# Performance work log

Hardware: AMD Instinct MI355X
Metric: run time of the kernel (lower is better)

Reference implementation:

```python
import jax, jax.numpy as jnp
import numpy as np

C = 16          # image channels (scaled from 1 for production-scale traffic)
GX = 36         # CORTIAL_WIDTH_COUNT
GY = 36         # CORTIAL_HEIGHT_COUNT
RF = 24         # receptive field size
IMG = 64        # image H = W
GAMMA_E = 0.9
GAMMA_I = 0.9


def setup_inputs() -> dict:
    key = jax.random.key(0)
    ks = jax.random.split(key, 7)
    x = jax.random.normal(ks[0], (C, IMG, IMG), dtype=jnp.float32)
    prev_activity = jax.random.uniform(ks[1], (C, GX, GY), dtype=jnp.float32)
    afferent_weights = jax.random.normal(ks[2], (C, GX, GY, RF, RF), dtype=jnp.float32) * 0.05
    ex_lateral_weights = jax.random.normal(ks[3], (C, GX, GY, GX, GY), dtype=jnp.float32) * 0.05
    in_lateral_weights = jax.random.normal(ks[4], (C, GX, GY, GX, GY), dtype=jnp.float32) * 0.05
    rx = jnp.sort(jax.random.randint(ks[5], (GX,), 0, IMG - RF + 1, dtype=jnp.int32))
    ry = jnp.sort(jax.random.randint(ks[6], (GY,), 0, IMG - RF + 1, dtype=jnp.int32))
    return {
        "x": x,
        "prev_activity": prev_activity,
        "afferent_weights": afferent_weights,
        "ex_lateral_weights": ex_lateral_weights,
        "in_lateral_weights": in_lateral_weights,
        "rx": rx,
        "ry": ry,
    }


def reference(x, prev_activity, afferent_weights, ex_lateral_weights, in_lateral_weights, rx, ry):
    # Gather all receptive-field patches at once: patches[c,i,j,u,v] = x[c, rx[i]+u, ry[j]+v]
    u = jnp.arange(RF)
    ix = (rx[:, None] + u)[:, None, :, None]   # [GX,1,RF,1]
    iy = (ry[:, None] + u)[None, :, None, :]   # [1,GY,1,RF]
    patches = x[:, ix, iy]                     # [C,GX,GY,RF,RF]

    # afferent_activation[:,i,j] = sum(patch * W_a[:,i,j]) (scalar broadcast across channels)
    aff = jnp.einsum('cijuv,cijuv->ij', patches, afferent_weights)
    # lateral activations: sum(prev[:,i,j] * W[:,i,j]) over all elements
    exc = jnp.einsum('cij,cijxy->ij', prev_activity, ex_lateral_weights)
    inh = jnp.einsum('cij,cijxy->ij', prev_activity, in_lateral_weights)

    total = aff + GAMMA_E * exc - GAMMA_I * inh   # [GX,GY]
    activity = jnp.maximum(total, 0.0)            # clamp(min=0) sigmoid approximation
    return jnp.broadcast_to(activity[None, :, :], (C, GX, GY))
```

## Files before the change

kernel.cpp:

```cpp
#include <hip/hip_runtime.h>


constexpr int C   = 16;
constexpr int GX  = 36;
constexpr int GY  = 36;
constexpr int RF  = 24;
constexpr int IMG = 64;
constexpr int GG  = GX * GY;
constexpr int RR  = RF * RF;
constexpr int SPLIT = 4;
constexpr int CPB   = C / SPLIT;

typedef float f4 __attribute__((ext_vector_type(4)));

__global__ __launch_bounds__(256)
void cortex_phase1(const float* __restrict__ x,
                   const float* __restrict__ prev,
                   const float* __restrict__ affW,
                   const float* __restrict__ exW,
                   const float* __restrict__ inW,
                   const int*   __restrict__ rx,
                   const int*   __restrict__ ry,
                   float* __restrict__ partial)
{
    const int bid   = blockIdx.x;
    const int ij    = bid % GG;
    const int split = bid / GG;
    const int cs    = split * CPB;
    const int i = ij / GY;
    const int j = ij - i * GY;
    const int t = threadIdx.x;

    const int rxi = rx[i];
    const int ryj = ry[j];

    float acc = 0.0f;

    if (t < RR / 4) {
        const int u  = t / (RF / 4);
        const int v0 = 4 * (t - u * (RF / 4));
        f4 w[CPB];
        #pragma unroll
        for (int cc = 0; cc < CPB; ++cc) {
            const int c = cs + cc;
            w[cc] = __builtin_nontemporal_load(
                (const f4*)(affW + ((size_t)c * GG + ij) * RR) + t);
        }
        #pragma unroll
        for (int cc = 0; cc < CPB; ++cc) {
            const int c = cs + cc;
            const float* xp = x + ((c * IMG + rxi + u) * IMG + ryj + v0);
            acc = fmaf(w[cc].x, xp[0], acc);
            acc = fmaf(w[cc].y, xp[1], acc);
            acc = fmaf(w[cc].z, xp[2], acc);
            acc = fmaf(w[cc].w, xp[3], acc);
        }
    }

    float d[CPB] = {0.0f, 0.0f, 0.0f, 0.0f};
    for (int k = t; k < GG / 4; k += 256) {
        f4 e[CPB], h[CPB];
        #pragma unroll
        for (int cc = 0; cc < CPB; ++cc) {
            const size_t base = ((size_t)(cs + cc) * GG + ij) * GG;
            e[cc] = __builtin_nontemporal_load((const f4*)(exW + base) + k);
            h[cc] = __builtin_nontemporal_load((const f4*)(inW + base) + k);
        }
        #pragma unroll
        for (int cc = 0; cc < CPB; ++cc)
            d[cc] += (e[cc].x + e[cc].y + e[cc].z + e[cc].w)
                   - (h[cc].x + h[cc].y + h[cc].z + h[cc].w);
    }
    {
        float lat = 0.0f;
        #pragma unroll
        for (int cc = 0; cc < CPB; ++cc)
            lat = fmaf(prev[(cs + cc) * GG + ij], d[cc], lat);
        acc = fmaf(0.9f, lat, acc);
    }

    for (int off = 32; off > 0; off >>= 1)
        acc += __shfl_down(acc, off, 64);

    __shared__ float sred[4];
    const int wave = t >> 6;
    const int lane = t & 63;
    if (lane == 0) sred[wave] = acc;
    __syncthreads();
    if (t == 0)
        partial[split * GG + ij] = sred[0] + sred[1] + sred[2] + sred[3];
}

__global__ __launch_bounds__(256)
void cortex_phase2(const float* __restrict__ partial, float* __restrict__ out)
{
    const int ij = blockIdx.x * blockDim.x + threadIdx.x;
    if (ij < GG) {
        const float tot = partial[ij] + partial[GG + ij]
                        + partial[2 * GG + ij] + partial[3 * GG + ij];
        const float a = fmaxf(tot, 0.0f);
        #pragma unroll
        for (int c = 0; c < C; ++c)
            out[c * GG + ij] = a;
    }
}

extern "C" void kernel_launch(void* const* d_in, const int* in_sizes, int n_in,
                              void* d_out, int out_size, void* d_ws, size_t ws_size,
                              hipStream_t stream) {
    const float* x     = (const float*)d_in[0];
    const float* prev  = (const float*)d_in[1];
    const float* affW  = (const float*)d_in[2];
    const float* exW   = (const float*)d_in[3];
    const float* inW   = (const float*)d_in[4];
    const int*   rx    = (const int*)d_in[5];
    const int*   ry    = (const int*)d_in[6];
    float* out     = (float*)d_out;
    float* partial = (float*)d_ws;

    cortex_phase1<<<GG * SPLIT, 256, 0, stream>>>(x, prev, affW, exW, inW, rx, ry, partial);
    cortex_phase2<<<(GG + 255) / 256, 256, 0, stream>>>(partial, out);
}
```

Baseline: 245.9 us.

## Flatten per-block work into uniform thread-strided loops with fewer channel splits

Halves the channel split so each block handles 8 channels, and flattens the afferent and lateral loads into one index space spread across all 256 threads instead of leaving most threads idle in the afferent part. Per-row pointers and signed prev-scaled coefficients are precomputed in shared memory, so excitatory and inhibitory rows are handled by one loop with eight independent 16-byte loads in flight per thread. This is meant to improve memory-level parallelism and lane utilization on a bandwidth-bound kernel, at the cost of integer divisions, a shared-memory sync and fewer blocks.

```diff
diff --git a/kernel.cpp b/kernel.cpp
--- a/kernel.cpp
+++ b/kernel.cpp
@@ -8,7 +8,7 @@
 constexpr int IMG = 64;
 constexpr int GG  = GX * GY;
 constexpr int RR  = RF * RF;
-constexpr int SPLIT = 4;
+constexpr int SPLIT = 2;
 constexpr int CPB   = C / SPLIT;
 
 typedef float f4 __attribute__((ext_vector_type(4)));
@@ -23,60 +23,78 @@
                    const int*   __restrict__ ry,
                    float* __restrict__ partial)
 {
-    const int bid   = blockIdx.x;
-    const int ij    = bid % GG;
-    const int split = bid / GG;
-    const int cs    = split * CPB;
+    const int bid  = blockIdx.x;
+    const int ij   = bid % GG;
+    const int half = bid / GG;
+    const int cs   = half * CPB;
     const int i = ij / GY;
     const int j = ij - i * GY;
-    const int t = threadIdx.x;
+    const unsigned t = threadIdx.x;
 
     const int rxi = rx[i];
     const int ryj = ry[j];
 
+    __shared__ float        s_co[2 * CPB];
+    __shared__ const float* s_rp[2 * CPB];
+    if (t < 2 * CPB) {
+        const int c = cs + (int)(t >> 1);
+        s_co[t] = prev[c * GG + ij] * ((t & 1u) ? -0.9f : 0.9f);
+        const float* base = (t & 1u) ? inW : exW;
+        s_rp[t] = base + ((size_t)c * GG + ij) * (size_t)GG;
+    }
+    __syncthreads();
+
     float acc = 0.0f;
 
-    if (t < RR / 4) {
-        const int u  = t / (RF / 4);
-        const int v0 = 4 * (t - u * (RF / 4));
-        f4 w[CPB];
+    {
+        constexpr unsigned NAF = CPB * RR / 4;
+        f4 w[5];
         #pragma unroll
-        for (int cc = 0; cc < CPB; ++cc) {
-            const int c = cs + cc;
-            w[cc] = __builtin_nontemporal_load(
-                (const f4*)(affW + ((size_t)c * GG + ij) * RR) + t);
+        for (int m = 0; m < 5; ++m) {
+            unsigned k = t + m * 256u;
+            if (k >= NAF) k = 0u;
+            const unsigned cl  = k / 144u;
+            const unsigned col = k - cl * 144u;
+            w[m] = __builtin_nontemporal_load(
+                (const f4*)(affW + ((size_t)(cs + cl) * GG + ij) * RR) + col);
         }
         #pragma unroll
-        for (int cc = 0; cc < CPB; ++cc) {
-            const int c = cs + cc;
-            const float* xp = x + ((c * IMG + rxi + u) * IMG + ryj + v0);
-            acc = fmaf(w[cc].x, xp[0], acc);
-            acc = fmaf(w[cc].y, xp[1], acc);
-            acc = fmaf(w[cc].z, xp[2], acc);
-            acc = fmaf(w[cc].w, xp[3], acc);
+        for (int m = 0; m < 5; ++m) {
+            const unsigned k = t + m * 256u;
+            if (k >= NAF) continue;
+            const unsigned cl  = k / 144u;
+            const unsigned col = k - cl * 144u;
+            const unsigned u   = col / 6u;
+            const unsigned v0  = (col - u * 6u) * 4u;
+            const float* xp = x + (((cs + cl) * IMG + rxi + u) * IMG + ryj + v0);
+            acc = fmaf(w[m].x, xp[0], acc);
+            acc = fmaf(w[m].y, xp[1], acc);
+            acc = fmaf(w[m].z, xp[2], acc);
+            acc = fmaf(w[m].w, xp[3], acc);
         }
     }
 
-    float d[CPB] = {0.0f, 0.0f, 0.0f, 0.0f};
-    for (int k = t; k < GG / 4; k += 256) {
-        f4 e[CPB], h[CPB];
-        #pragma unroll
-        for (int cc = 0; cc < CPB; ++cc) {
-            const size_t base = ((size_t)(cs + cc) * GG + ij) * GG;
-            e[cc] = __builtin_nontemporal_load((const f4*)(exW + base) + k);
-            h[cc] = __builtin_nontemporal_load((const f4*)(inW + base) + k);
+    {
+        constexpr unsigned NLAT = 2 * CPB * (GG / 4);
+        for (unsigned base = 0; base < NLAT; base += 8 * 256) {
+            f4    v[8];
+            float cf[8];
+            #pragma unroll
+            for (int m = 0; m < 8; ++m) {
+                unsigned k = base + m * 256u + t;
+                if (k >= NLAT) k = 0u;
+                const unsigned r   = k / 324u;
+                const unsigned col = k - r * 324u;
+                v[m]  = __builtin_nontemporal_load((const f4*)s_rp[r] + col);
+                cf[m] = s_co[r];
+            }
+            #pragma unroll
+            for (int m = 0; m < 8; ++m) {
+                const unsigned k = base + m * 256u + t;
+                const float cfm = (k < NLAT) ? cf[m] : 0.0f;
+                acc = fmaf(cfm, (v[m].x + v[m].y) + (v[m].z + v[m].w), acc);
+            }
         }
-        #pragma unroll
-        for (int cc = 0; cc < CPB; ++cc)
-            d[cc] += (e[cc].x + e[cc].y + e[cc].z + e[cc].w)
-                   - (h[cc].x + h[cc].y + h[cc].z + h[cc].w);
-    }
-    {
-        float lat = 0.0f;
-        #pragma unroll
-        for (int cc = 0; cc < CPB; ++cc)
-            lat = fmaf(prev[(cs + cc) * GG + ij], d[cc], lat);
-        acc = fmaf(0.9f, lat, acc);
     }
 
     for (int off = 32; off > 0; off >>= 1)
@@ -88,7 +106,7 @@
     if (lane == 0) sred[wave] = acc;
     __syncthreads();
     if (t == 0)
-        partial[split * GG + ij] = sred[0] + sred[1] + sred[2] + sred[3];
+        partial[half * GG + ij] = sred[0] + sred[1] + sred[2] + sred[3];
 }
 
 __global__ __launch_bounds__(256)
@@ -96,8 +114,7 @@
 {
     const int ij = blockIdx.x * blockDim.x + threadIdx.x;
     if (ij < GG) {
-        const float tot = partial[ij] + partial[GG + ij]
-                        + partial[2 * GG + ij] + partial[3 * GG + ij];
+        const float tot = partial[ij] + partial[GG + ij];
         const float a = fmaxf(tot, 0.0f);
         #pragma unroll
         for (int c = 0; c < C; ++c)
```

Measured after the change: 247.5 us. Within noise of the previous version (+0.7%).

## Fuse split-channel reduction into one kernel using atomic last-block finalize

Applied to the files above, without the earlier changes.

Merges the two-phase launch into a single kernel. The last of the SPLIT blocks for each output cell, found through an atomic counter, sums the partials, applies ReLU and writes all channels. A memset to zero the counters replaces the second kernel launch. It also switches the afferent weight loads from nontemporal to ordinary loads. The aim is to remove one launch and the gap between kernels, in exchange for atomic traffic and a memset.

```diff
diff --git a/kernel.cpp b/kernel.cpp
--- a/kernel.cpp
+++ b/kernel.cpp
@@ -14,14 +14,16 @@
 typedef float f4 __attribute__((ext_vector_type(4)));
 
 __global__ __launch_bounds__(256)
-void cortex_phase1(const float* __restrict__ x,
-                   const float* __restrict__ prev,
-                   const float* __restrict__ affW,
-                   const float* __restrict__ exW,
-                   const float* __restrict__ inW,
-                   const int*   __restrict__ rx,
-                   const int*   __restrict__ ry,
-                   float* __restrict__ partial)
+void cortex_fused(const float* __restrict__ x,
+                  const float* __restrict__ prev,
+                  const float* __restrict__ affW,
+                  const float* __restrict__ exW,
+                  const float* __restrict__ inW,
+                  const int*   __restrict__ rx,
+                  const int*   __restrict__ ry,
+                  float* __restrict__ partial,
+                  int*   __restrict__ cnt,
+                  float* __restrict__ out)
 {
     const int bid   = blockIdx.x;
     const int ij    = bid % GG;
@@ -43,8 +45,7 @@
         #pragma unroll
         for (int cc = 0; cc < CPB; ++cc) {
             const int c = cs + cc;
-            w[cc] = __builtin_nontemporal_load(
-                (const f4*)(affW + ((size_t)c * GG + ij) * RR) + t);
+            w[cc] = ((const f4*)(affW + ((size_t)c * GG + ij) * RR))[t];
         }
         #pragma unroll
         for (int cc = 0; cc < CPB; ++cc) {
@@ -87,21 +88,24 @@
     const int lane = t & 63;
     if (lane == 0) sred[wave] = acc;
     __syncthreads();
-    if (t == 0)
-        partial[split * GG + ij] = sred[0] + sred[1] + sred[2] + sred[3];
-}
 
-__global__ __launch_bounds__(256)
-void cortex_phase2(const float* __restrict__ partial, float* __restrict__ out)
-{
-    const int ij = blockIdx.x * blockDim.x + threadIdx.x;
-    if (ij < GG) {
-        const float tot = partial[ij] + partial[GG + ij]
-                        + partial[2 * GG + ij] + partial[3 * GG + ij];
-        const float a = fmaxf(tot, 0.0f);
-        #pragma unroll
-        for (int c = 0; c < C; ++c)
-            out[c * GG + ij] = a;
+    if (t == 0) {
+        const float psum = sred[0] + sred[1] + sred[2] + sred[3];
+        __hip_atomic_store(&partial[split * GG + ij], psum,
+                           __ATOMIC_RELEASE, __HIP_MEMORY_SCOPE_AGENT);
+        const int prevCnt = __hip_atomic_fetch_add(&cnt[ij], 1,
+                           __ATOMIC_ACQ_REL, __HIP_MEMORY_SCOPE_AGENT);
+        if (prevCnt == SPLIT - 1) {
+            float tot = 0.0f;
+            #pragma unroll
+            for (int s = 0; s < SPLIT; ++s)
+                tot += __hip_atomic_load(&partial[s * GG + ij],
+                           __ATOMIC_RELAXED, __HIP_MEMORY_SCOPE_AGENT);
+            const float a = fmaxf(tot, 0.0f);
+            #pragma unroll
+            for (int c = 0; c < C; ++c)
+                out[c * GG + ij] = a;
+        }
     }
 }
 
@@ -115,9 +119,12 @@
     const float* inW   = (const float*)d_in[4];
     const int*   rx    = (const int*)d_in[5];
     const int*   ry    = (const int*)d_in[6];
-    float* out     = (float*)d_out;
+    float* out = (float*)d_out;
+
     float* partial = (float*)d_ws;
+    int*   cnt     = (int*)((char*)d_ws + SPLIT * GG * sizeof(float));
 
-    cortex_phase1<<<GG * SPLIT, 256, 0, stream>>>(x, prev, affW, exW, inW, rx, ry, partial);
-    cortex_phase2<<<(GG + 255) / 256, 256, 0, stream>>>(partial, out);
+    hipMemsetAsync(cnt, 0, GG * sizeof(int), stream);
+    cortex_fused<<<GG * SPLIT, 256, 0, stream>>>(x, prev, affW, exW, inW,
+                                                 rx, ry, partial, cnt, out);
 }
```

Result: slower. 704.1 us (+186.3%).
